# Kernel optimization log

Hardware: AMD Instinct MI355X
Metric: run time of the kernel (lower is better)

The kernel has to match this reference:

```python
import jax, jax.numpy as jnp
import numpy as np

B, INPUT, N, M, H, OUT = 128, 128, 4096, 128, 512, 128
EPS = 1e-8


def setup_inputs() -> dict:
    key = jax.random.key(0)
    ks = jax.random.split(key, 17)
    rn = lambda i, shape, s=1.0: jax.random.normal(ks[i], shape, dtype=jnp.float32) * s
    sm = lambda x: jax.nn.softmax(x, axis=-1)
    return {
        "inp": rn(0, (B, INPUT)),
        "prev_reads": rn(1, (B, M), 0.01),
        "h_prev": rn(2, (B, H), 0.1),
        "c_prev": rn(3, (B, H), 0.1),
        "prev_read_weights": sm(rn(4, (B, N))),
        "prev_write_weights": sm(rn(5, (B, N))),
        "memory": rn(6, (B, N, M), 0.05),
        "W_ih": rn(7, (4 * H, INPUT + M), 0.02),
        "W_hh": rn(8, (4 * H, H), 0.02),
        "b_ih": jnp.zeros((4 * H,), jnp.float32),
        "b_hh": jnp.zeros((4 * H,), jnp.float32),
        "read_W": rn(9, (H, M + 6), 0.05),
        "read_b": jnp.zeros((M + 6,), jnp.float32),
        "write_W": rn(10, (H, 3 * M + 6), 0.05),
        "write_b": jnp.zeros((3 * M + 6,), jnp.float32),
        "fc_W": rn(11, (H + M, OUT), 0.05),
        "fc_b": rn(12, (OUT,), 0.01),
    }


def _lstm_cell(x, h, c, W_ih, W_hh, b_ih, b_hh):
    gates = x @ W_ih.T + h @ W_hh.T + b_ih + b_hh  # [B,4H]
    i, f, g, o = jnp.split(gates, 4, axis=-1)      # torch LSTMCell gate order
    c_new = jax.nn.sigmoid(f) * c + jax.nn.sigmoid(i) * jnp.tanh(g)
    h_new = jax.nn.sigmoid(o) * jnp.tanh(c_new)
    return h_new, c_new


def _address(memory, prev_w, k, beta, g, s, gamma):
    # content addressing: cosine similarity of key k [B,M] vs memory [B,N,M]
    dot = jnp.einsum("bnm,bm->bn", memory, k)
    norm = jnp.linalg.norm(memory, axis=-1) * jnp.linalg.norm(k, axis=-1, keepdims=True)
    sim = dot / (norm + EPS)
    w_c = jax.nn.softmax(beta[:, None] * sim, axis=-1)          # [B,N]
    w_g = g[:, None] * w_c + (1.0 - g[:, None]) * prev_w        # interpolation
    # circular convolution with 3-tap shift distribution s [B,3] (shifts -1,0,+1)
    w_t = (s[:, 0:1] * jnp.roll(w_g, 1, axis=1)
           + s[:, 1:2] * w_g
           + s[:, 2:3] * jnp.roll(w_g, -1, axis=1))
    # sharpening
    w_sh = (w_t + EPS) ** gamma[:, None]
    return w_sh / jnp.sum(w_sh, axis=-1, keepdims=True)


def _split_addr(p):
    k = jnp.tanh(p[:, :M])
    beta = jax.nn.softplus(p[:, M])
    g = jax.nn.sigmoid(p[:, M + 1])
    s = jax.nn.softmax(p[:, M + 2:M + 5], axis=-1)
    gamma = 1.0 + jax.nn.softplus(p[:, M + 5])
    return k, beta, g, s, gamma


def reference(inp, prev_reads, h_prev, c_prev, prev_read_weights, prev_write_weights,
              memory, W_ih, W_hh, b_ih, b_hh, read_W, read_b, write_W, write_b,
              fc_W, fc_b):
    # controller step on cat([inp] + prev_reads)
    x = jnp.concatenate([inp, prev_reads], axis=1)
    h, c = _lstm_cell(x, h_prev, c_prev, W_ih, W_hh, b_ih, b_hh)

    # read head: address then read (memory before any write, per original loop order)
    rp = h @ read_W + read_b
    read_w = _address(memory, prev_read_weights, *_split_addr(rp))
    read_vec = jnp.einsum("bn,bnm->bm", read_w, memory)

    # write head: address, then erase/add
    wp = h @ write_W + write_b
    write_w = _address(memory, prev_write_weights, *_split_addr(wp[:, :M + 6]))
    e = jax.nn.sigmoid(wp[:, M + 6:2 * M + 6])
    a = jnp.tanh(wp[:, 2 * M + 6:])
    w3 = write_w[:, :, None]
    new_memory = memory * (1.0 - w3 * e[:, None, :]) + w3 * a[:, None, :]

    out = jax.nn.sigmoid(jnp.concatenate([h, read_vec], axis=1) @ fc_W + fc_b)
    return (out, read_vec, h, c, read_w, write_w, new_memory)
```

## Files before the change

kernel.cpp:

```cpp
#include <hip/hip_runtime.h>
#include <math.h>

#define B_ 128
#define INPUT_ 128
#define N_ 4096
#define M_ 128
#define H_ 512
#define OUT_ 128
#define EPS_ 1e-8f

typedef float f4v __attribute__((ext_vector_type(4)));

#define OUT_OFF    0
#define RV_OUT_OFF 16384
#define H_OFF      32768
#define C_OFF      98304
#define RW_OFF     163840
#define WW_OFF     688128
#define NM_OFF     1212416

#define KR_OFF     0
#define KW_OFF     16384
#define E_OFF      32768
#define A_OFF      49152
#define PRR_OFF    65536
#define PRW_OFF    66560
#define SIMR_OFF   67584
#define SIMW_OFF   591872
#define RVACC_OFF  1116160
#define PART_OFF   1132544

#define KSPLIT 8
#define KPER   96
#define BO     64

#define J_FULL 524
#define J_PAD  576
#define KS2    4

__device__ __forceinline__ float sigmoidf_(float x){ return 1.0f/(1.0f+expf(-x)); }
__device__ __forceinline__ float softplusf_(float x){ return fmaxf(x,0.0f) + log1pf(expf(-fabsf(x))); }

__global__ __launch_bounds__(256) void k1a_gemm(
    const float* __restrict__ inp, const float* __restrict__ prev_reads,
    const float* __restrict__ h_prev,
    const float* __restrict__ W_ih, const float* __restrict__ W_hh,
    float* __restrict__ part)
{
  __shared__ float wt[32*68];
  __shared__ float xs[32*128];
  int t = threadIdx.x;
  int O0 = blockIdx.x * BO;
  int ks = blockIdx.y;
  int oq = t >> 5, bq = t & 31;
  float acc[8][4];
  #pragma unroll
  for (int i=0;i<8;++i)
    #pragma unroll
    for (int c=0;c<4;++c) acc[i][c]=0.f;

  for (int st = 0; st < 3; ++st) {
    int kg0 = ks*KPER + st*32;
    __syncthreads();
    {
      int o = t >> 2, kq = t & 3;
      int j = O0 + o;
      const float* wsrc; int col;
      if (kg0 < 256) { wsrc = W_ih + (size_t)j*256; col = kg0; }
      else           { wsrc = W_hh + (size_t)j*512; col = kg0 - 256; }
      float4 a0 = *(const float4*)(wsrc + col + kq*8);
      float4 a1 = *(const float4*)(wsrc + col + kq*8 + 4);
      int kk = kq*8;
      wt[(kk+0)*68+o]=a0.x; wt[(kk+1)*68+o]=a0.y; wt[(kk+2)*68+o]=a0.z; wt[(kk+3)*68+o]=a0.w;
      wt[(kk+4)*68+o]=a1.x; wt[(kk+5)*68+o]=a1.y; wt[(kk+6)*68+o]=a1.z; wt[(kk+7)*68+o]=a1.w;
    }
    {
      int b = t >> 1, kq = t & 1;
      const float* src; int col;
      if (kg0 < 128)      { src = inp        + (size_t)b*128; col = kg0; }
      else if (kg0 < 256) { src = prev_reads + (size_t)b*128; col = kg0-128; }
      else                { src = h_prev     + (size_t)b*512; col = kg0-256; }
      #pragma unroll
      for (int r = 0; r < 4; ++r) {
        float4 v = *(const float4*)(src + col + kq*16 + r*4);
        int kk = kq*16 + r*4;
        xs[(kk+0)*128+b]=v.x; xs[(kk+1)*128+b]=v.y; xs[(kk+2)*128+b]=v.z; xs[(kk+3)*128+b]=v.w;
      }
    }
    __syncthreads();
    #pragma unroll
    for (int kk = 0; kk < 32; ++kk) {
      float4 wa = *(const float4*)&wt[kk*68 + oq*8];
      float4 wb = *(const float4*)&wt[kk*68 + oq*8 + 4];
      float4 xv = *(const float4*)&xs[kk*128 + bq*4];
      float wv[8] = {wa.x,wa.y,wa.z,wa.w,wb.x,wb.y,wb.z,wb.w};
      float xx[4] = {xv.x,xv.y,xv.z,xv.w};
      #pragma unroll
      for (int i=0;i<8;++i)
        #pragma unroll
        for (int c=0;c<4;++c)
          acc[i][c] += wv[i]*xx[c];
    }
  }
  #pragma unroll
  for (int i=0;i<8;++i) {
    int j = O0 + oq*8 + i;
    float4 v = make_float4(acc[i][0],acc[i][1],acc[i][2],acc[i][3]);
    *(float4*)(part + ((size_t)ks*2048 + j)*128 + bq*4) = v;
  }
}

__global__ __launch_bounds__(128) void k1b_act(
    const float* __restrict__ part, const float* __restrict__ c_prev,
    const float* __restrict__ b_ih, const float* __restrict__ b_hh,
    float* __restrict__ h_out, float* __restrict__ c_out)
{
  int u = blockIdx.x;
  int b = threadIdx.x;
  float g[4];
  #pragma unroll
  for (int q=0;q<4;++q) {
    int j = q*H_ + u;
    float s = b_ih[j] + b_hh[j];
    #pragma unroll
    for (int ksp=0;ksp<KSPLIT;++ksp)
      s += part[((size_t)ksp*2048 + j)*128 + b];
    g[q] = s;
  }
  float ig = sigmoidf_(g[0]), fg = sigmoidf_(g[1]);
  float gg = tanhf(g[2]),     og = sigmoidf_(g[3]);
  float cn = fg * c_prev[(size_t)b*H_ + u] + ig*gg;
  float hn = og * tanhf(cn);
  c_out[(size_t)b*H_ + u] = cn;
  h_out[(size_t)b*H_ + u] = hn;
}

__global__ __launch_bounds__(256) void k2a_gemm(
    const float* __restrict__ h,
    const float* __restrict__ read_W, const float* __restrict__ write_W,
    float* __restrict__ part)
{
  __shared__ float wt[32*68];
  __shared__ float xs[32*128];
  int t = threadIdx.x;
  int j0 = blockIdx.x * 64;
  int ks = blockIdx.y;
  int jq = t >> 5, bq = t & 31;
  float acc[8][4];
  #pragma unroll
  for (int i=0;i<8;++i)
    #pragma unroll
    for (int c=0;c<4;++c) acc[i][c]=0.f;

  for (int st = 0; st < 4; ++st) {
    int k0 = ks*128 + st*32;
    __syncthreads();
    for (int e = t; e < 32*64; e += 256) {
      int kk = e >> 6, j = e & 63;
      int jc = j0 + j;
      int u = k0 + kk;
      float v = 0.f;
      if (jc < 134)          v = read_W[(size_t)u*134 + jc];
      else if (jc < J_FULL)  v = write_W[(size_t)u*390 + (jc-134)];
      wt[kk*68 + j] = v;
    }
    {
      int b = t >> 1, kq = t & 1;
      const float* src = h + (size_t)b*512 + k0 + kq*16;
      #pragma unroll
      for (int r = 0; r < 4; ++r) {
        float4 v = *(const float4*)(src + r*4);
        int kk = kq*16 + r*4;
        xs[(kk+0)*128+b]=v.x; xs[(kk+1)*128+b]=v.y; xs[(kk+2)*128+b]=v.z; xs[(kk+3)*128+b]=v.w;
      }
    }
    __syncthreads();
    #pragma unroll
    for (int kk = 0; kk < 32; ++kk) {
      float4 wa = *(const float4*)&wt[kk*68 + jq*8];
      float4 wb = *(const float4*)&wt[kk*68 + jq*8 + 4];
      float4 xv = *(const float4*)&xs[kk*128 + bq*4];
      float wv[8] = {wa.x,wa.y,wa.z,wa.w,wb.x,wb.y,wb.z,wb.w};
      float xx[4] = {xv.x,xv.y,xv.z,xv.w};
      #pragma unroll
      for (int i=0;i<8;++i)
        #pragma unroll
        for (int c=0;c<4;++c)
          acc[i][c] += wv[i]*xx[c];
    }
  }
  #pragma unroll
  for (int c=0;c<4;++c) {
    int b = bq*4 + c;
    float4 v0 = make_float4(acc[0][c],acc[1][c],acc[2][c],acc[3][c]);
    float4 v1 = make_float4(acc[4][c],acc[5][c],acc[6][c],acc[7][c]);
    *(float4*)(part + ((size_t)ks*128 + b)*J_PAD + j0 + jq*8)     = v0;
    *(float4*)(part + ((size_t)ks*128 + b)*J_PAD + j0 + jq*8 + 4) = v1;
  }
}

__global__ __launch_bounds__(256) void k2b_post(
    const float* __restrict__ part,
    const float* __restrict__ read_b, const float* __restrict__ write_b,
    float* __restrict__ ws)
{
  int b = blockIdx.x, t = threadIdx.x;
  __shared__ float raw[J_FULL];
  __shared__ float red[128];
  for (int j = t; j < J_FULL; j += 256) {
    float s = (j < 134) ? read_b[j] : write_b[j-134];
    #pragma unroll
    for (int ks = 0; ks < KS2; ++ks)
      s += part[((size_t)ks*128 + b)*J_PAD + j];
    raw[j] = s;
  }
  __syncthreads();
  float krv = 0.f, kwv = 0.f;
  if (t < 128) {
    krv = tanhf(raw[t]);
    kwv = tanhf(raw[134+t]);
    ws[KR_OFF + b*M_ + t] = krv;
    ws[KW_OFF + b*M_ + t] = kwv;
    ws[E_OFF  + b*M_ + t] = sigmoidf_(raw[268+t]);
    ws[A_OFF  + b*M_ + t] = tanhf(raw[396+t]);
  }
  if (t < 128) red[t] = krv*krv;
  __syncthreads();
  for (int s = 64; s > 0; s >>= 1) { if (t < s) red[t] += red[t+s]; __syncthreads(); }
  float nr = sqrtf(red[0]);
  __syncthreads();
  if (t < 128) red[t] = kwv*kwv;
  __syncthreads();
  for (int s = 64; s > 0; s >>= 1) { if (t < s) red[t] += red[t+s]; __syncthreads(); }
  float nw = sqrtf(red[0]);
  if (t == 0) {
    float beta = softplusf_(raw[128]);
    float g    = sigmoidf_(raw[129]);
    float s0 = raw[130], s1 = raw[131], s2 = raw[132];
    float mx = fmaxf(s0, fmaxf(s1, s2));
    float e0 = expf(s0-mx), e1 = expf(s1-mx), e2 = expf(s2-mx);
    float es = e0+e1+e2;
    float gamma = 1.0f + softplusf_(raw[133]);
    float* pr = ws + PRR_OFF + b*8;
    pr[0]=beta; pr[1]=g; pr[2]=gamma; pr[3]=e0/es; pr[4]=e1/es; pr[5]=e2/es; pr[6]=nr;
  }
  if (t == 1) {
    float beta = softplusf_(raw[262]);
    float g    = sigmoidf_(raw[263]);
    float s0 = raw[264], s1 = raw[265], s2 = raw[266];
    float mx = fmaxf(s0, fmaxf(s1, s2));
    float e0 = expf(s0-mx), e1 = expf(s1-mx), e2 = expf(s2-mx);
    float es = e0+e1+e2;
    float gamma = 1.0f + softplusf_(raw[267]);
    float* pr = ws + PRW_OFF + b*8;
    pr[0]=beta; pr[1]=g; pr[2]=gamma; pr[3]=e0/es; pr[4]=e1/es; pr[5]=e2/es; pr[6]=nw;
  }
}

__global__ __launch_bounds__(256) void k3_sim(const float* __restrict__ memory,
                                              float* __restrict__ ws)
{
  int b = blockIdx.y, t = threadIdx.x;
  int n0 = blockIdx.x * 64;
  __shared__ float skr[128], skw[128];
  if (t < 128) { skr[t] = ws[KR_OFF + b*M_ + t]; skw[t] = ws[KW_OFF + b*M_ + t]; }
  __syncthreads();
  float knr = ws[PRR_OFF + b*8 + 6];
  float knw = ws[PRW_OFF + b*8 + 6];
  int wave = t >> 6, lane = t & 63, half = lane >> 5, l32 = lane & 31;
  int m0 = l32 * 4;
  #pragma unroll
  for (int i = 0; i < 8; ++i) {
    int n = n0 + i*8 + wave*2 + half;
    const float4* row = (const float4*)(memory + ((size_t)b*N_ + n)*M_);
    float4 v = row[l32];
    float dr = v.x*skr[m0] + v.y*skr[m0+1] + v.z*skr[m0+2] + v.w*skr[m0+3];
    float dw = v.x*skw[m0] + v.y*skw[m0+1] + v.z*skw[m0+2] + v.w*skw[m0+3];
    float ss = v.x*v.x + v.y*v.y + v.z*v.z + v.w*v.w;
    #pragma unroll
    for (int msk = 16; msk >= 1; msk >>= 1) {
      dr += __shfl_xor(dr, msk, 64);
      dw += __shfl_xor(dw, msk, 64);
      ss += __shfl_xor(ss, msk, 64);
    }
    if (l32 == 0) {
      float nm = sqrtf(ss);
      ws[SIMR_OFF + (size_t)b*N_ + n] = dr / (nm*knr + EPS_);
      ws[SIMW_OFF + (size_t)b*N_ + n] = dw / (nm*knw + EPS_);
    }
  }
}

__global__ __launch_bounds__(512) void k4_addr(
    const float* __restrict__ prev_rw, const float* __restrict__ prev_ww,
    float* __restrict__ ws, float* __restrict__ d_out)
{
  int which = blockIdx.x, b = blockIdx.y, t = threadIdx.x;
  int wid = t >> 6, lane = t & 63;
  const float* sim  = ws + (which ? SIMW_OFF : SIMR_OFF) + (size_t)b*N_;
  const float* prev = (which ? prev_ww : prev_rw) + (size_t)b*N_;
  const float* pr   = ws + (which ? PRW_OFF : PRR_OFF) + b*8;
  float* outw = d_out + (which ? WW_OFF : RW_OFF) + (size_t)b*N_;
  float beta = pr[0], g = pr[1], gamma = pr[2], s0 = pr[3], s1 = pr[4], s2 = pr[5];

  __shared__ float w[N_];
  __shared__ float redmax[8], redsum[8], redp[8];

  float vv[8];
  float mx = -1e30f;
  #pragma unroll
  for (int k = 0; k < 8; ++k) {
    int i = t + k*512;
    float v = beta * sim[i];
    vv[k] = v;
    mx = fmaxf(mx, v);
  }
  #pragma unroll
  for (int m = 1; m <= 32; m <<= 1) mx = fmaxf(mx, __shfl_xor(mx, m, 64));
  if (lane == 0) redmax[wid] = mx;
  __syncthreads();
  mx = redmax[0];
  #pragma unroll
  for (int j = 1; j < 8; ++j) mx = fmaxf(mx, redmax[j]);

  float sum = 0.f;
  #pragma unroll
  for (int k = 0; k < 8; ++k) {
    float v = __expf(vv[k] - mx);
    vv[k] = v;
    sum += v;
  }
  #pragma unroll
  for (int m = 1; m <= 32; m <<= 1) sum += __shfl_xor(sum, m, 64);
  if (lane == 0) redsum[wid] = sum;
  __syncthreads();
  sum = 0.f;
  #pragma unroll
  for (int j = 0; j < 8; ++j) sum += redsum[j];
  float inv = 1.0f / sum;

  #pragma unroll
  for (int k = 0; k < 8; ++k) {
    int i = t + k*512;
    w[i] = g * vv[k] * inv + (1.0f - g) * prev[i];
  }
  __syncthreads();

  float p[8]; float psum = 0.f;
  #pragma unroll
  for (int k = 0; k < 8; ++k) {
    int i = t + k*512;
    float wt = s0 * w[(i-1)&(N_-1)] + s1 * w[i] + s2 * w[(i+1)&(N_-1)];
    float v = __expf(gamma * __logf(wt + EPS_));
    p[k] = v; psum += v;
  }
  #pragma unroll
  for (int m = 1; m <= 32; m <<= 1) psum += __shfl_xor(psum, m, 64);
  if (lane == 0) redp[wid] = psum;
  __syncthreads();
  psum = 0.f;
  #pragma unroll
  for (int j = 0; j < 8; ++j) psum += redp[j];
  float pinv = 1.0f / psum;
  #pragma unroll
  for (int k = 0; k < 8; ++k) {
    int i = t + k*512;
    outw[i] = p[k] * pinv;
  }
}

__global__ __launch_bounds__(256) void k5_update(
    const float* __restrict__ memory, float* __restrict__ d_out,
    float* __restrict__ ws, float* __restrict__ rvp)
{
  int br = 127 - blockIdx.y;
  int txr = 63 - blockIdx.x;
  int t = threadIdx.x;
  int n0 = txr * 64;
  __shared__ float se[128], sa[128];
  __shared__ float rvsh[8][128];
  if (t < 128) {
    se[t] = ws[E_OFF + br*M_ + t];
    sa[t] = ws[A_OFF + br*M_ + t];
  }
  __syncthreads();
  const float* rw  = d_out + RW_OFF + (size_t)br*N_;
  const float* wwp = d_out + WW_OFF + (size_t)br*N_;
  float* nm = d_out + NM_OFF;
  int wave = t >> 6, lane = t & 63, half = lane >> 5, l32 = lane & 31;
  int slot = wave*2 + half;
  int m0 = l32 * 4;
  float rx = 0.f, ry = 0.f, rz = 0.f, rw4 = 0.f;
  #pragma unroll
  for (int i = 0; i < 8; ++i) {
    int n = n0 + i*8 + slot;
    size_t off = ((size_t)br*N_ + n) * M_;
    f4v v = __builtin_nontemporal_load((const f4v*)(memory + off) + l32);
    float rwn = rw[n], wwn = wwp[n];
    rx += rwn*v.x; ry += rwn*v.y; rz += rwn*v.z; rw4 += rwn*v.w;
    f4v o;
    o.x = v.x * (1.0f - wwn*se[m0+0]) + wwn*sa[m0+0];
    o.y = v.y * (1.0f - wwn*se[m0+1]) + wwn*sa[m0+1];
    o.z = v.z * (1.0f - wwn*se[m0+2]) + wwn*sa[m0+2];
    o.w = v.w * (1.0f - wwn*se[m0+3]) + wwn*sa[m0+3];
    __builtin_nontemporal_store(o, (f4v*)(nm + off) + l32);
  }
  rvsh[slot][m0+0] = rx;
  rvsh[slot][m0+1] = ry;
  rvsh[slot][m0+2] = rz;
  rvsh[slot][m0+3] = rw4;
  __syncthreads();
  if (t < 128) {
    float s = 0.f;
    #pragma unroll
    for (int j = 0; j < 8; ++j) s += rvsh[j][t];
    rvp[((size_t)br*64 + txr)*128 + t] = s;
  }
}

__global__ __launch_bounds__(128) void k6_fc(
    const float* __restrict__ fc_W, const float* __restrict__ fc_b,
    float* __restrict__ d_out, const float* __restrict__ rvp)
{
  int b = blockIdx.x, t = threadIdx.x;
  __shared__ float xh[H_ + M_];
  for (int i = t; i < H_; i += 128) xh[i] = d_out[H_OFF + b*H_ + i];
  float rv = 0.f;
  #pragma unroll 8
  for (int tile = 0; tile < 64; ++tile)
    rv += rvp[((size_t)b*64 + tile)*128 + t];
  xh[H_ + t] = rv;
  d_out[RV_OUT_OFF + b*M_ + t] = rv;
  __syncthreads();
  float acc = fc_b[t];
  for (int j = 0; j < H_ + M_; ++j) acc += xh[j] * fc_W[j*OUT_ + t];
  d_out[OUT_OFF + b*OUT_ + t] = sigmoidf_(acc);
}

extern "C" void kernel_launch(void* const* d_in, const int* in_sizes, int n_in,
                              void* d_out, int out_size, void* d_ws, size_t ws_size,
                              hipStream_t stream)
{
  const float* inp        = (const float*)d_in[0];
  const float* prev_reads = (const float*)d_in[1];
  const float* h_prev     = (const float*)d_in[2];
  const float* c_prev     = (const float*)d_in[3];
  const float* prev_rw    = (const float*)d_in[4];
  const float* prev_ww    = (const float*)d_in[5];
  const float* memory     = (const float*)d_in[6];
  const float* W_ih       = (const float*)d_in[7];
  const float* W_hh       = (const float*)d_in[8];
  const float* b_ih       = (const float*)d_in[9];
  const float* b_hh       = (const float*)d_in[10];
  const float* read_W     = (const float*)d_in[11];
  const float* read_b     = (const float*)d_in[12];
  const float* write_W    = (const float*)d_in[13];
  const float* write_b    = (const float*)d_in[14];
  const float* fc_W       = (const float*)d_in[15];
  const float* fc_b       = (const float*)d_in[16];
  float* out = (float*)d_out;
  float* ws  = (float*)d_ws;

  k1a_gemm<<<dim3(32, KSPLIT), 256, 0, stream>>>(inp, prev_reads, h_prev,
                                                 W_ih, W_hh, ws + PART_OFF);
  k1b_act<<<512, 128, 0, stream>>>(ws + PART_OFF, c_prev, b_ih, b_hh,
                                   out + H_OFF, out + C_OFF);
  k2a_gemm<<<dim3(9, KS2), 256, 0, stream>>>(out + H_OFF, read_W, write_W,
                                             ws + PART_OFF);
  k2b_post<<<B_, 256, 0, stream>>>(ws + PART_OFF, read_b, write_b, ws);
  k3_sim<<<dim3(64, B_), 256, 0, stream>>>(memory, ws);
  k4_addr<<<dim3(2, B_), 512, 0, stream>>>(prev_rw, prev_ww, ws, out);
  k5_update<<<dim3(64, B_), 256, 0, stream>>>(memory, out, ws, ws + PART_OFF);
  k6_fc<<<B_, 128, 0, stream>>>(fc_W, fc_b, out, ws + PART_OFF);
}
```

Measured before the change: 209.9 us.

## Fuse similarity and addressing via last-block counter; batch-group memory passes for L2 reuse

Merges the cosine-similarity kernel and the addressing kernel into one. An atomic per-batch counter lets the last of the 64 tiles run the softmax, shift and sharpen for that batch, which removes a separate launch. The memory-bound sim and update kernels are also launched in groups of 32 batches, so the second read of each group's memory slice (about 64 MB) may still hit the large last-level cache. The cost is a serialized tail where a single block handles addressing per batch, more launches, and an extra memset.

```diff
diff --git a/kernel.cpp b/kernel.cpp
--- a/kernel.cpp
+++ b/kernel.cpp
@@ -27,7 +27,7 @@
 #define PRW_OFF    66560
 #define SIMR_OFF   67584
 #define SIMW_OFF   591872
-#define RVACC_OFF  1116160
+#define CNT_OFF    1116160
 #define PART_OFF   1132544
 
 #define KSPLIT 8
@@ -37,6 +37,8 @@
 #define J_FULL 524
 #define J_PAD  576
 #define KS2    4
+
+#define GRP    32
 
 __device__ __forceinline__ float sigmoidf_(float x){ return 1.0f/(1.0f+expf(-x)); }
 __device__ __forceinline__ float softplusf_(float x){ return fmaxf(x,0.0f) + log1pf(expf(-fabsf(x))); }
@@ -257,13 +259,20 @@
   }
 }
 
-__global__ __launch_bounds__(256) void k3_sim(const float* __restrict__ memory,
-                                              float* __restrict__ ws)
-{
-  int b = blockIdx.y, t = threadIdx.x;
+__global__ __launch_bounds__(256) void k3k4(
+    const float* __restrict__ memory,
+    const float* __restrict__ prev_rw, const float* __restrict__ prev_ww,
+    float* __restrict__ ws, float* __restrict__ d_out,
+    unsigned* __restrict__ cnt, int b0)
+{
+  int b = b0 + blockIdx.y;
+  int t = threadIdx.x;
   int n0 = blockIdx.x * 64;
-  __shared__ float skr[128], skw[128];
-  if (t < 128) { skr[t] = ws[KR_OFF + b*M_ + t]; skw[t] = ws[KW_OFF + b*M_ + t]; }
+  __shared__ float sh[N_];
+  __shared__ float red[8];
+  __shared__ unsigned done_s;
+
+  if (t < 128) { sh[t] = ws[KR_OFF + b*M_ + t]; sh[128+t] = ws[KW_OFF + b*M_ + t]; }
   __syncthreads();
   float knr = ws[PRR_OFF + b*8 + 6];
   float knw = ws[PRW_OFF + b*8 + 6];
@@ -274,8 +283,8 @@
     int n = n0 + i*8 + wave*2 + half;
     const float4* row = (const float4*)(memory + ((size_t)b*N_ + n)*M_);
     float4 v = row[l32];
-    float dr = v.x*skr[m0] + v.y*skr[m0+1] + v.z*skr[m0+2] + v.w*skr[m0+3];
-    float dw = v.x*skw[m0] + v.y*skw[m0+1] + v.z*skw[m0+2] + v.w*skw[m0+3];
+    float dr = v.x*sh[m0] + v.y*sh[m0+1] + v.z*sh[m0+2] + v.w*sh[m0+3];
+    float dw = v.x*sh[128+m0] + v.y*sh[128+m0+1] + v.z*sh[128+m0+2] + v.w*sh[128+m0+3];
     float ss = v.x*v.x + v.y*v.y + v.z*v.z + v.w*v.w;
     #pragma unroll
     for (int msk = 16; msk >= 1; msk >>= 1) {
@@ -289,103 +298,93 @@
       ws[SIMW_OFF + (size_t)b*N_ + n] = dw / (nm*knw + EPS_);
     }
   }
-}
-
-__global__ __launch_bounds__(512) void k4_addr(
-    const float* __restrict__ prev_rw, const float* __restrict__ prev_ww,
-    float* __restrict__ ws, float* __restrict__ d_out)
-{
-  int which = blockIdx.x, b = blockIdx.y, t = threadIdx.x;
-  int wid = t >> 6, lane = t & 63;
-  const float* sim  = ws + (which ? SIMW_OFF : SIMR_OFF) + (size_t)b*N_;
-  const float* prev = (which ? prev_ww : prev_rw) + (size_t)b*N_;
-  const float* pr   = ws + (which ? PRW_OFF : PRR_OFF) + b*8;
-  float* outw = d_out + (which ? WW_OFF : RW_OFF) + (size_t)b*N_;
-  float beta = pr[0], g = pr[1], gamma = pr[2], s0 = pr[3], s1 = pr[4], s2 = pr[5];
-
-  __shared__ float w[N_];
-  __shared__ float redmax[8], redsum[8], redp[8];
-
-  float vv[8];
-  float mx = -1e30f;
-  #pragma unroll
-  for (int k = 0; k < 8; ++k) {
-    int i = t + k*512;
-    float v = beta * sim[i];
-    vv[k] = v;
-    mx = fmaxf(mx, v);
-  }
-  #pragma unroll
-  for (int m = 1; m <= 32; m <<= 1) mx = fmaxf(mx, __shfl_xor(mx, m, 64));
-  if (lane == 0) redmax[wid] = mx;
-  __syncthreads();
-  mx = redmax[0];
-  #pragma unroll
-  for (int j = 1; j < 8; ++j) mx = fmaxf(mx, redmax[j]);
-
-  float sum = 0.f;
-  #pragma unroll
-  for (int k = 0; k < 8; ++k) {
-    float v = __expf(vv[k] - mx);
-    vv[k] = v;
-    sum += v;
-  }
-  #pragma unroll
-  for (int m = 1; m <= 32; m <<= 1) sum += __shfl_xor(sum, m, 64);
-  if (lane == 0) redsum[wid] = sum;
-  __syncthreads();
-  sum = 0.f;
-  #pragma unroll
-  for (int j = 0; j < 8; ++j) sum += redsum[j];
-  float inv = 1.0f / sum;
-
-  #pragma unroll
-  for (int k = 0; k < 8; ++k) {
-    int i = t + k*512;
-    w[i] = g * vv[k] * inv + (1.0f - g) * prev[i];
-  }
-  __syncthreads();
-
-  float p[8]; float psum = 0.f;
-  #pragma unroll
-  for (int k = 0; k < 8; ++k) {
-    int i = t + k*512;
-    float wt = s0 * w[(i-1)&(N_-1)] + s1 * w[i] + s2 * w[(i+1)&(N_-1)];
-    float v = __expf(gamma * __logf(wt + EPS_));
-    p[k] = v; psum += v;
-  }
-  #pragma unroll
-  for (int m = 1; m <= 32; m <<= 1) psum += __shfl_xor(psum, m, 64);
-  if (lane == 0) redp[wid] = psum;
-  __syncthreads();
-  psum = 0.f;
-  #pragma unroll
-  for (int j = 0; j < 8; ++j) psum += redp[j];
-  float pinv = 1.0f / psum;
-  #pragma unroll
-  for (int k = 0; k < 8; ++k) {
-    int i = t + k*512;
-    outw[i] = p[k] * pinv;
+
+  __syncthreads();
+  if (t == 0)
+    done_s = __hip_atomic_fetch_add(&cnt[b], 1u, __ATOMIC_ACQ_REL, __HIP_MEMORY_SCOPE_AGENT);
+  __syncthreads();
+  if (done_s != 63) return;
+
+  for (int which = 0; which < 2; ++which) {
+    const float* sim  = ws + (which ? SIMW_OFF : SIMR_OFF) + (size_t)b*N_;
+    const float* prev = (which ? prev_ww : prev_rw) + (size_t)b*N_;
+    const float* pr   = ws + (which ? PRW_OFF : PRR_OFF) + b*8;
+    float* outw = d_out + (which ? WW_OFF : RW_OFF) + (size_t)b*N_;
+    float beta = pr[0], g = pr[1], gamma = pr[2], s0 = pr[3], s1 = pr[4], s2 = pr[5];
+
+    float vv[16];
+    float mx = -1e30f;
+    #pragma unroll
+    for (int k = 0; k < 16; ++k) {
+      float v = beta * sim[t + k*256];
+      vv[k] = v;
+      mx = fmaxf(mx, v);
+    }
+    #pragma unroll
+    for (int m = 1; m <= 32; m <<= 1) mx = fmaxf(mx, __shfl_xor(mx, m, 64));
+    if (lane == 0) red[wave] = mx;
+    __syncthreads();
+    mx = fmaxf(fmaxf(red[0], red[1]), fmaxf(red[2], red[3]));
+
+    float sum = 0.f;
+    #pragma unroll
+    for (int k = 0; k < 16; ++k) {
+      float v = __expf(vv[k] - mx);
+      vv[k] = v; sum += v;
+    }
+    #pragma unroll
+    for (int m = 1; m <= 32; m <<= 1) sum += __shfl_xor(sum, m, 64);
+    __syncthreads();
+    if (lane == 0) red[wave] = sum;
+    __syncthreads();
+    float inv = 1.0f / (red[0] + red[1] + red[2] + red[3]);
+
+    __syncthreads();
+    #pragma unroll
+    for (int k = 0; k < 16; ++k) {
+      int i = t + k*256;
+      sh[i] = g * vv[k] * inv + (1.0f - g) * prev[i];
+    }
+    __syncthreads();
+
+    float psum = 0.f;
+    #pragma unroll
+    for (int k = 0; k < 16; ++k) {
+      int i = t + k*256;
+      float wt = s0 * sh[(i-1)&(N_-1)] + s1 * sh[i] + s2 * sh[(i+1)&(N_-1)];
+      float v = __expf(gamma * __logf(wt + EPS_));
+      vv[k] = v; psum += v;
+    }
+    #pragma unroll
+    for (int m = 1; m <= 32; m <<= 1) psum += __shfl_xor(psum, m, 64);
+    __syncthreads();
+    if (lane == 0) red[wave] = psum;
+    __syncthreads();
+    float pinv = 1.0f / (red[0] + red[1] + red[2] + red[3]);
+    #pragma unroll
+    for (int k = 0; k < 16; ++k)
+      outw[t + k*256] = vv[k] * pinv;
+    __syncthreads();
   }
 }
 
 __global__ __launch_bounds__(256) void k5_update(
     const float* __restrict__ memory, float* __restrict__ d_out,
-    float* __restrict__ ws, float* __restrict__ rvp)
-{
-  int br = 127 - blockIdx.y;
-  int txr = 63 - blockIdx.x;
+    float* __restrict__ ws, float* __restrict__ rvp, int b0)
+{
+  int b = b0 + blockIdx.y;
+  int tx = blockIdx.x;
   int t = threadIdx.x;
-  int n0 = txr * 64;
+  int n0 = tx * 64;
   __shared__ float se[128], sa[128];
   __shared__ float rvsh[8][128];
   if (t < 128) {
-    se[t] = ws[E_OFF + br*M_ + t];
-    sa[t] = ws[A_OFF + br*M_ + t];
-  }
-  __syncthreads();
-  const float* rw  = d_out + RW_OFF + (size_t)br*N_;
-  const float* wwp = d_out + WW_OFF + (size_t)br*N_;
+    se[t] = ws[E_OFF + b*M_ + t];
+    sa[t] = ws[A_OFF + b*M_ + t];
+  }
+  __syncthreads();
+  const float* rw  = d_out + RW_OFF + (size_t)b*N_;
+  const float* wwp = d_out + WW_OFF + (size_t)b*N_;
   float* nm = d_out + NM_OFF;
   int wave = t >> 6, lane = t & 63, half = lane >> 5, l32 = lane & 31;
   int slot = wave*2 + half;
@@ -394,7 +393,7 @@
   #pragma unroll
   for (int i = 0; i < 8; ++i) {
     int n = n0 + i*8 + slot;
-    size_t off = ((size_t)br*N_ + n) * M_;
+    size_t off = ((size_t)b*N_ + n) * M_;
     f4v v = __builtin_nontemporal_load((const f4v*)(memory + off) + l32);
     float rwn = rw[n], wwn = wwp[n];
     rx += rwn*v.x; ry += rwn*v.y; rz += rwn*v.z; rw4 += rwn*v.w;
@@ -414,7 +413,7 @@
     float s = 0.f;
     #pragma unroll
     for (int j = 0; j < 8; ++j) s += rvsh[j][t];
-    rvp[((size_t)br*64 + txr)*128 + t] = s;
+    rvp[((size_t)b*64 + tx)*128 + t] = s;
   }
 }
 
@@ -461,6 +460,7 @@
   float* out = (float*)d_out;
   float* ws  = (float*)d_ws;
 
+  hipMemsetAsync(ws + CNT_OFF, 0, B_*sizeof(unsigned), stream);
   k1a_gemm<<<dim3(32, KSPLIT), 256, 0, stream>>>(inp, prev_reads, h_prev,
                                                  W_ih, W_hh, ws + PART_OFF);
   k1b_act<<<512, 128, 0, stream>>>(ws + PART_OFF, c_prev, b_ih, b_hh,
@@ -468,8 +468,11 @@
   k2a_gemm<<<dim3(9, KS2), 256, 0, stream>>>(out + H_OFF, read_W, write_W,
                                              ws + PART_OFF);
   k2b_post<<<B_, 256, 0, stream>>>(ws + PART_OFF, read_b, write_b, ws);
-  k3_sim<<<dim3(64, B_), 256, 0, stream>>>(memory, ws);
-  k4_addr<<<dim3(2, B_), 512, 0, stream>>>(prev_rw, prev_ww, ws, out);
-  k5_update<<<dim3(64, B_), 256, 0, stream>>>(memory, out, ws, ws + PART_OFF);
+  for (int g = 0; g < B_ / GRP; ++g) {
+    k3k4<<<dim3(64, GRP), 256, 0, stream>>>(memory, prev_rw, prev_ww, ws, out,
+                                            (unsigned*)(ws + CNT_OFF), g*GRP);
+    k5_update<<<dim3(64, GRP), 256, 0, stream>>>(memory, out, ws,
+                                                 ws + PART_OFF, g*GRP);
+  }
   k6_fc<<<B_, 128, 0, stream>>>(fc_W, fc_b, out, ws + PART_OFF);
 }
```

Result: slower. 581.9 us (+177.3%).

## Stage memory as bf16 copy in sim kernel and read it in update kernel

Applied to the files above, without the earlier changes.

The similarity kernel now also writes a bf16-rounded copy of the memory tensor into extra workspace. When the workspace is large enough, the update kernel reads that half-size copy instead of the fp32 memory to produce new_memory and the read partials. The fc kernel now handles four batch rows per block, reusing each fc_W load across those rows. This trades an extra 128MB write for a smaller read in the update kernel. It also rounds memory values to bf16 before the erase/add and read, which loses precision in the outputs.

```diff
diff --git a/kernel.cpp b/kernel.cpp
--- a/kernel.cpp
+++ b/kernel.cpp
@@ -29,6 +29,8 @@
 #define SIMW_OFF   591872
 #define RVACC_OFF  1116160
 #define PART_OFF   1132544
+#define WS_BASE_FLOATS 3229696ull
+#define BF_BYTES   134217728ull
 
 #define KSPLIT 8
 #define KPER   96
@@ -40,6 +42,14 @@
 
 __device__ __forceinline__ float sigmoidf_(float x){ return 1.0f/(1.0f+expf(-x)); }
 __device__ __forceinline__ float softplusf_(float x){ return fmaxf(x,0.0f) + log1pf(expf(-fabsf(x))); }
+__device__ __forceinline__ unsigned short f2bf_(float x){
+  union { float f; unsigned u; } c; c.f = x;
+  unsigned u = c.u + 0x7FFFu + ((c.u >> 16) & 1u);
+  return (unsigned short)(u >> 16);
+}
+__device__ __forceinline__ float bf2f_(unsigned short h){
+  union { unsigned u; float f; } c; c.u = ((unsigned)h) << 16; return c.f;
+}
 
 __global__ __launch_bounds__(256) void k1a_gemm(
     const float* __restrict__ inp, const float* __restrict__ prev_reads,
@@ -258,7 +268,8 @@
 }
 
 __global__ __launch_bounds__(256) void k3_sim(const float* __restrict__ memory,
-                                              float* __restrict__ ws)
+                                              float* __restrict__ ws,
+                                              unsigned short* __restrict__ bf)
 {
   int b = blockIdx.y, t = threadIdx.x;
   int n0 = blockIdx.x * 64;
@@ -274,6 +285,11 @@
     int n = n0 + i*8 + wave*2 + half;
     const float4* row = (const float4*)(memory + ((size_t)b*N_ + n)*M_);
     float4 v = row[l32];
+    if (bf) {
+      ushort4 us;
+      us.x = f2bf_(v.x); us.y = f2bf_(v.y); us.z = f2bf_(v.z); us.w = f2bf_(v.w);
+      *((ushort4*)(bf + ((size_t)b*N_ + n)*M_) + l32) = us;
+    }
     float dr = v.x*skr[m0] + v.y*skr[m0+1] + v.z*skr[m0+2] + v.w*skr[m0+3];
     float dw = v.x*skw[m0] + v.y*skw[m0+1] + v.z*skw[m0+2] + v.w*skw[m0+3];
     float ss = v.x*v.x + v.y*v.y + v.z*v.z + v.w*v.w;
@@ -369,7 +385,57 @@
   }
 }
 
-__global__ __launch_bounds__(256) void k5_update(
+__global__ __launch_bounds__(256) void k5_update_bf(
+    const unsigned short* __restrict__ bfm, float* __restrict__ d_out,
+    float* __restrict__ ws, float* __restrict__ rvp)
+{
+  int br = 127 - blockIdx.y;
+  int txr = 63 - blockIdx.x;
+  int t = threadIdx.x;
+  int n0 = txr * 64;
+  __shared__ float se[128], sa[128];
+  __shared__ float rvsh[8][128];
+  if (t < 128) {
+    se[t] = ws[E_OFF + br*M_ + t];
+    sa[t] = ws[A_OFF + br*M_ + t];
+  }
+  __syncthreads();
+  const float* rw  = d_out + RW_OFF + (size_t)br*N_;
+  const float* wwp = d_out + WW_OFF + (size_t)br*N_;
+  float* nm = d_out + NM_OFF;
+  int wave = t >> 6, lane = t & 63, half = lane >> 5, l32 = lane & 31;
+  int slot = wave*2 + half;
+  int m0 = l32 * 4;
+  float rx = 0.f, ry = 0.f, rz = 0.f, rw4 = 0.f;
+  #pragma unroll
+  for (int i = 0; i < 8; ++i) {
+    int n = n0 + i*8 + slot;
+    size_t off = ((size_t)br*N_ + n) * M_;
+    ushort4 us = *((const ushort4*)(bfm + off) + l32);
+    float vx = bf2f_(us.x), vy = bf2f_(us.y), vz = bf2f_(us.z), vw = bf2f_(us.w);
+    float rwn = rw[n], wwn = wwp[n];
+    rx += rwn*vx; ry += rwn*vy; rz += rwn*vz; rw4 += rwn*vw;
+    f4v o;
+    o.x = vx * (1.0f - wwn*se[m0+0]) + wwn*sa[m0+0];
+    o.y = vy * (1.0f - wwn*se[m0+1]) + wwn*sa[m0+1];
+    o.z = vz * (1.0f - wwn*se[m0+2]) + wwn*sa[m0+2];
+    o.w = vw * (1.0f - wwn*se[m0+3]) + wwn*sa[m0+3];
+    __builtin_nontemporal_store(o, (f4v*)(nm + off) + l32);
+  }
+  rvsh[slot][m0+0] = rx;
+  rvsh[slot][m0+1] = ry;
+  rvsh[slot][m0+2] = rz;
+  rvsh[slot][m0+3] = rw4;
+  __syncthreads();
+  if (t < 128) {
+    float s = 0.f;
+    #pragma unroll
+    for (int j = 0; j < 8; ++j) s += rvsh[j][t];
+    rvp[((size_t)br*64 + txr)*128 + t] = s;
+  }
+}
+
+__global__ __launch_bounds__(256) void k5_update_f32(
     const float* __restrict__ memory, float* __restrict__ d_out,
     float* __restrict__ ws, float* __restrict__ rvp)
 {
@@ -422,19 +488,32 @@
     const float* __restrict__ fc_W, const float* __restrict__ fc_b,
     float* __restrict__ d_out, const float* __restrict__ rvp)
 {
-  int b = blockIdx.x, t = threadIdx.x;
-  __shared__ float xh[H_ + M_];
-  for (int i = t; i < H_; i += 128) xh[i] = d_out[H_OFF + b*H_ + i];
-  float rv = 0.f;
-  #pragma unroll 8
-  for (int tile = 0; tile < 64; ++tile)
-    rv += rvp[((size_t)b*64 + tile)*128 + t];
-  xh[H_ + t] = rv;
-  d_out[RV_OUT_OFF + b*M_ + t] = rv;
-  __syncthreads();
-  float acc = fc_b[t];
-  for (int j = 0; j < H_ + M_; ++j) acc += xh[j] * fc_W[j*OUT_ + t];
-  d_out[OUT_OFF + b*OUT_ + t] = sigmoidf_(acc);
+  int b0 = blockIdx.x * 4, t = threadIdx.x;
+  __shared__ float xh[4][H_ + M_];
+  #pragma unroll
+  for (int q = 0; q < 4; ++q)
+    for (int i = t; i < H_; i += 128)
+      xh[q][i] = d_out[H_OFF + (size_t)(b0+q)*H_ + i];
+  #pragma unroll
+  for (int q = 0; q < 4; ++q) {
+    float rv = 0.f;
+    #pragma unroll 8
+    for (int tile = 0; tile < 64; ++tile)
+      rv += rvp[((size_t)(b0+q)*64 + tile)*128 + t];
+    xh[q][H_ + t] = rv;
+    d_out[RV_OUT_OFF + (size_t)(b0+q)*M_ + t] = rv;
+  }
+  __syncthreads();
+  float bias = fc_b[t];
+  float a0 = bias, a1 = bias, a2 = bias, a3 = bias;
+  for (int j = 0; j < H_ + M_; ++j) {
+    float w = fc_W[(size_t)j*OUT_ + t];
+    a0 += xh[0][j]*w; a1 += xh[1][j]*w; a2 += xh[2][j]*w; a3 += xh[3][j]*w;
+  }
+  d_out[OUT_OFF + (size_t)(b0+0)*OUT_ + t] = sigmoidf_(a0);
+  d_out[OUT_OFF + (size_t)(b0+1)*OUT_ + t] = sigmoidf_(a1);
+  d_out[OUT_OFF + (size_t)(b0+2)*OUT_ + t] = sigmoidf_(a2);
+  d_out[OUT_OFF + (size_t)(b0+3)*OUT_ + t] = sigmoidf_(a3);
 }
 
 extern "C" void kernel_launch(void* const* d_in, const int* in_sizes, int n_in,
@@ -461,6 +540,10 @@
   float* out = (float*)d_out;
   float* ws  = (float*)d_ws;
 
+  bool fast = ws_size >= WS_BASE_FLOATS*4ull + BF_BYTES;
+  unsigned short* bfm = fast
+      ? (unsigned short*)((char*)d_ws + WS_BASE_FLOATS*4ull) : (unsigned short*)0;
+
   k1a_gemm<<<dim3(32, KSPLIT), 256, 0, stream>>>(inp, prev_reads, h_prev,
                                                  W_ih, W_hh, ws + PART_OFF);
   k1b_act<<<512, 128, 0, stream>>>(ws + PART_OFF, c_prev, b_ih, b_hh,
@@ -468,8 +551,11 @@
   k2a_gemm<<<dim3(9, KS2), 256, 0, stream>>>(out + H_OFF, read_W, write_W,
                                              ws + PART_OFF);
   k2b_post<<<B_, 256, 0, stream>>>(ws + PART_OFF, read_b, write_b, ws);
-  k3_sim<<<dim3(64, B_), 256, 0, stream>>>(memory, ws);
+  k3_sim<<<dim3(64, B_), 256, 0, stream>>>(memory, ws, bfm);
   k4_addr<<<dim3(2, B_), 512, 0, stream>>>(prev_rw, prev_ww, ws, out);
-  k5_update<<<dim3(64, B_), 256, 0, stream>>>(memory, out, ws, ws + PART_OFF);
-  k6_fc<<<B_, 128, 0, stream>>>(fc_W, fc_b, out, ws + PART_OFF);
-}
+  if (fast)
+    k5_update_bf<<<dim3(64, B_), 256, 0, stream>>>(bfm, out, ws, ws + PART_OFF);
+  else
+    k5_update_f32<<<dim3(64, B_), 256, 0, stream>>>(memory, out, ws, ws + PART_OFF);
+  k6_fc<<<B_/4, 128, 0, stream>>>(fc_W, fc_b, out, ws + PART_OFF);
+}
```

Measured after the change: 249.4 us. 18.9% more time.
